# Performance work log

Measured on AMD Instinct MI355X. Metric: run time of the kernel, lower is better.

The kernel has to match this reference:

```python
import jax, jax.numpy as jnp
import numpy as np

N_NODES = 50000
N_EDGES = 200000
N_GRAPHS = 64
BN_EPS = 1e-5


def _gat(x, src, dst, W, a_src, a_dst, b, heads, ch, concat):
    # x: [N, F_in] -> h: [N, H, C]
    N = x.shape[0]
    h = (x @ W).reshape(N, heads, ch)
    alpha_s = jnp.sum(h * a_src, axis=-1)  # [N, H]
    alpha_d = jnp.sum(h * a_dst, axis=-1)  # [N, H]
    e = jax.nn.leaky_relu(alpha_s[src] + alpha_d[dst], 0.2)  # [E, H]
    # segment softmax over destination nodes
    m = jax.ops.segment_max(e, dst, num_segments=N)  # [N, H]
    e = jnp.exp(e - m[dst])
    s = jax.ops.segment_sum(e, dst, num_segments=N)
    alpha = e / (s[dst] + 1e-16)  # [E, H]
    msg = h[src] * alpha[:, :, None]  # [E, H, C]
    out = jax.ops.segment_sum(msg, dst, num_segments=N)  # [N, H, C]
    out = out.reshape(N, heads * ch) if concat else out.mean(axis=1)
    return out + b


def _bn(x, gamma, beta):
    # eval-mode BatchNorm1d with running_mean=0, running_var=1
    return x * (gamma / jnp.sqrt(1.0 + BN_EPS)) + beta


def _mlp3(g, W1, b1, W2, b2, W3, b3):
    h = jax.nn.relu(g @ W1 + b1)
    h = jax.nn.relu(h @ W2 + b2)
    return h @ W3 + b3


def setup_inputs() -> dict:
    key = jax.random.key(0)
    ks = jax.random.split(key, 48)
    it = iter(range(48))

    def nrm(shape, fan_in):
        return jax.random.normal(ks[next(it)], shape, jnp.float32) / np.sqrt(fan_in)

    x = jax.random.normal(ks[next(it)], (N_NODES, 62), jnp.float32)
    edge_index = jax.random.randint(ks[next(it)], (2, N_EDGES), 0, N_NODES, jnp.int32)
    batch = jnp.sort(jax.random.randint(ks[next(it)], (N_NODES,), 0, N_GRAPHS, jnp.int32))

    d = dict(x=x, edge_index=edge_index, batch=batch)
    d.update(
        Win=nrm((62, 256), 62), b_in=jnp.zeros((256,), jnp.float32),
        W1=nrm((256, 1024), 256), as1=nrm((8, 128), 128), ad1=nrm((8, 128), 128),
        b1=jnp.zeros((1024,), jnp.float32), g1=jnp.ones((1024,), jnp.float32), be1=jnp.zeros((1024,), jnp.float32),
        W2=nrm((1024, 1024), 1024), as2=nrm((8, 128), 128), ad2=nrm((8, 128), 128),
        b2=jnp.zeros((1024,), jnp.float32), g2=jnp.ones((1024,), jnp.float32), be2=jnp.zeros((1024,), jnp.float32),
        W3=nrm((1024, 1024), 1024), as3=nrm((4, 256), 256), ad3=nrm((4, 256), 256),
        b3=jnp.zeros((256,), jnp.float32), g3=jnp.ones((256,), jnp.float32), be3=jnp.zeros((256,), jnp.float32),
        Wp=nrm((768, 256), 768), bp=jnp.zeros((256,), jnp.float32),
        Wv1=nrm((256, 128), 256), bv1=jnp.zeros((128,), jnp.float32),
        Wv2=nrm((128, 64), 128), bv2=jnp.zeros((64,), jnp.float32),
        Wv3=nrm((64, 2), 64), bv3=jnp.zeros((2,), jnp.float32),
        Wt1=nrm((256, 128), 256), bt1=jnp.zeros((128,), jnp.float32),
        Wt2=nrm((128, 64), 128), bt2=jnp.zeros((64,), jnp.float32),
        Wt3=nrm((64, 10), 64), bt3=jnp.zeros((10,), jnp.float32),
        Wc1=nrm((256, 64), 256), bc1=jnp.zeros((64,), jnp.float32),
        Wc2=nrm((64, 1), 64), bc2=jnp.zeros((1,), jnp.float32),
    )
    return d


def reference(x, edge_index, batch, Win, b_in,
              W1, as1, ad1, b1, g1, be1,
              W2, as2, ad2, b2, g2, be2,
              W3, as3, ad3, b3, g3, be3,
              Wp, bp,
              Wv1, bv1, Wv2, bv2, Wv3, bv3,
              Wt1, bt1, Wt2, bt2, Wt3, bt3,
              Wc1, bc1, Wc2, bc2):
    N = x.shape[0]
    loop = jnp.arange(N, dtype=edge_index.dtype)
    src = jnp.concatenate([edge_index[0], loop])  # add_self_loops (PyG default)
    dst = jnp.concatenate([edge_index[1], loop])

    h = jax.nn.relu(x @ Win + b_in)
    x1 = jax.nn.relu(_bn(_gat(h, src, dst, W1, as1, ad1, b1, 8, 128, True), g1, be1))
    x2 = jax.nn.relu(_bn(_gat(x1, src, dst, W2, as2, ad2, b2, 8, 128, True), g2, be2))
    x3 = jax.nn.relu(_bn(_gat(x2, src, dst, W3, as3, ad3, b3, 4, 256, False), g3, be3))

    add_pool = jax.ops.segment_sum(x3, batch, num_segments=N_GRAPHS)
    cnt = jax.ops.segment_sum(jnp.ones((N,), x3.dtype), batch, num_segments=N_GRAPHS)
    mean_pool = add_pool / jnp.maximum(cnt, 1.0)[:, None]
    max_pool = jax.ops.segment_max(x3, batch, num_segments=N_GRAPHS)
    max_pool = jnp.where(jnp.isfinite(max_pool), max_pool, 0.0)

    pooled = jnp.concatenate([mean_pool, max_pool, add_pool], axis=1)  # [G, 768]
    g = jax.nn.relu(pooled @ Wp + bp)

    vuln = _mlp3(g, Wv1, bv1, Wv2, bv2, Wv3, bv3)            # [G, 2]
    vtype = _mlp3(g, Wt1, bt1, Wt2, bt2, Wt3, bt3)           # [G, 10]
    conf = jax.nn.sigmoid(jax.nn.relu(g @ Wc1 + bc1) @ Wc2 + bc2)  # [G, 1]
    return (vuln, vtype, conf)
```

## Files before the change

### kernel.cpp

```cpp
#include <hip/hip_runtime.h>
#include <stdint.h>

static constexpr int NN = 50000;
static constexpr int NP = 50176;
static constexpr int NE = 200000;
static constexpr int NG = 64;
#define BN_S 0.99999500003749968f

typedef __bf16 bf16x8 __attribute__((ext_vector_type(8)));
typedef float  f32x4  __attribute__((ext_vector_type(4)));
typedef __attribute__((address_space(1))) void* as1p;
typedef __attribute__((address_space(3))) void* as3p;
typedef unsigned short u16;

__device__ __forceinline__ float b2f(u16 u){ union{uint32_t i;float f;}x; x.i=((uint32_t)u)<<16; return x.f; }
__device__ __forceinline__ float lo_f(uint32_t u){ union{uint32_t i;float f;}x; x.i=u<<16; return x.f; }
__device__ __forceinline__ float hi_f(uint32_t u){ union{uint32_t i;float f;}x; x.i=u&0xffff0000u; return x.f; }
__device__ __forceinline__ u16 f2b(float f){
  union{float f;uint32_t i;}x; x.f=f;
  return (u16)((x.i + 0x7fffu + ((x.i>>16)&1u)) >> 16);
}
__device__ __forceinline__ void lds_cp16(const void* g, void* l){
  __builtin_amdgcn_global_load_lds((as1p)g, (as3p)l, 16, 0, 0);
}

__global__ void k_detect(const uint32_t* __restrict__ win, int* __restrict__ flag){
  const int lane = threadIdx.x;
  const uint32_t w = win[lane];
  const int e = (w >> 7) & 0xFF;
  const bool band = (e >= 100 && e <= 140) || ((w & 0xFFFFu) == 0u);
  unsigned long long m = __ballot(band);
  if (lane == 0) *flag = (__popcll(m) < 32) ? 1 : 0;
}

struct CvtJobs {
  const void* src[34];
  int n[34];
  int dstoff[34];
  int cum[35];
  int njobs;
  int total;
};
__global__ __launch_bounds__(256) void k_cvt(CvtJobs jobs, const int* __restrict__ flag,
                                             u16* __restrict__ dst0){
  const int i = blockIdx.x*256 + threadIdx.x;
  if (i >= jobs.total) return;
  int lo = 0, hi = jobs.njobs - 1;
  while (lo < hi){ int mid = (lo+hi+1)>>1; if (jobs.cum[mid] <= i) lo = mid; else hi = mid-1; }
  const int j = lo;
  const int e = i - jobs.cum[j];
  u16 v = (*flag) ? f2b(((const float*)jobs.src[j])[e]) : ((const u16*)jobs.src[j])[e];
  dst0[jobs.dstoff[j] + e] = v;
}

__global__ void k_pad_x(const void* __restrict__ x, u16* __restrict__ xp, const int* __restrict__ flag){
  int i = blockIdx.x*256 + threadIdx.x;
  if (i >= NP*64) return;
  int n = i >> 6, k = i & 63;
  u16 v = 0;
  if (n < NN && k < 62)
    v = (*flag) ? f2b(((const float*)x)[n*62 + k]) : ((const u16*)x)[n*62 + k];
  xp[i] = v;
}
__global__ void k_pad_winT(const void* __restrict__ w, u16* __restrict__ wt, const int* __restrict__ flag){
  int i = blockIdx.x*256 + threadIdx.x;
  if (i >= 256*64) return;
  int o = i >> 6, k = i & 63;
  u16 v = 0;
  if (k < 62)
    v = (*flag) ? f2b(((const float*)w)[k*256 + o]) : ((const u16*)w)[k*256 + o];
  wt[i] = v;
}
__global__ void k_transpose(const void* __restrict__ w, u16* __restrict__ wt, int K, int NO,
                            const int* __restrict__ flag){
  int i = blockIdx.x*256 + threadIdx.x;
  if (i >= K*NO) return;
  int k = i / NO, o = i - k*NO;
  u16 v = (*flag) ? f2b(((const float*)w)[i]) : ((const u16*)w)[i];
  wt[(size_t)o*K + k] = v;
}

__global__ void k_init_counts(int* counts){
  int i = blockIdx.x*256 + threadIdx.x;
  if (i < NN) counts[i] = 1;
}
__global__ void k_count(const int* __restrict__ eidx, int* counts){
  int e = blockIdx.x*256 + threadIdx.x;
  if (e < NE) atomicAdd(&counts[eidx[NE + e]], 1);
}
__global__ __launch_bounds__(1024) void k_scan(const int* __restrict__ counts,
                                               int* __restrict__ indptr, int* __restrict__ cursor){
  __shared__ int sums[1024];
  const int t = threadIdx.x;
  const int strip = (NN + 1023)/1024;
  int lo = t*strip, hi = lo+strip < NN ? lo+strip : NN;
  int s = 0;
  for (int i=lo;i<hi;i++) s += counts[i];
  sums[t] = s; __syncthreads();
  for (int off=1; off<1024; off<<=1){
    int v = (t>=off) ? sums[t-off] : 0;
    __syncthreads();
    sums[t] += v;
    __syncthreads();
  }
  int base = t ? sums[t-1] : 0;
  for (int i=lo;i<hi;i++){ indptr[i]=base; cursor[i]=base; base += counts[i]; }
  if (t == 1023) indptr[NN] = sums[1023];
}
__global__ void k_fill(const int* __restrict__ eidx, int* cursor, int* __restrict__ srcs){
  int i = blockIdx.x*256 + threadIdx.x;
  if (i >= NE + NN) return;
  int s, d;
  if (i < NE){ s = eidx[i]; d = eidx[NE+i]; }
  else { s = d = i - NE; }
  int p = atomicAdd(&cursor[d], 1);
  srcs[p] = s;
}

template<int K, bool EPI, int BNSH>
__global__ __launch_bounds__(256) void k_gemm_bt(const u16* __restrict__ A, const u16* __restrict__ B,
                                                 u16* __restrict__ C, int ldc, const u16* __restrict__ bias){
  __shared__ __align__(16) u16 As[128*64];
  __shared__ __align__(16) u16 Bs[128*64];
  const int tid = threadIdx.x;
  const int lane = tid & 63, wv = tid >> 6;
  const int bid = blockIdx.x;
  const size_t bm = bid >> BNSH, bn = bid & ((1<<BNSH)-1);
  const u16* Ab = A + bm*128*(size_t)K;
  const u16* Bb = B + bn*128*(size_t)K;
  f32x4 acc[4][4] = {};
  const int wm = (wv>>1)*64, wn = (wv&1)*64;
  const int r = lane & 15, kg = lane >> 4;
  const int srow = wv*32 + (lane>>3);
  const int scol = (lane&7)*8;
  for (int kt = 0; kt < K; kt += 64){
    #pragma unroll
    for (int i=0;i<4;i++){
      lds_cp16(Ab + (size_t)(srow + i*8)*K + kt + scol, (char*)As + (wv*4+i)*1024);
      lds_cp16(Bb + (size_t)(srow + i*8)*K + kt + scol, (char*)Bs + (wv*4+i)*1024);
    }
    __syncthreads();
    #pragma unroll
    for (int ks=0; ks<2; ks++){
      bf16x8 a[4], b[4];
      const int ko = ks*32 + kg*8;
      #pragma unroll
      for (int i=0;i<4;i++) a[i] = *(const bf16x8*)(As + (wm + i*16 + r)*64 + ko);
      #pragma unroll
      for (int j=0;j<4;j++) b[j] = *(const bf16x8*)(Bs + (wn + j*16 + r)*64 + ko);
      #pragma unroll
      for (int i=0;i<4;i++)
        #pragma unroll
        for (int j=0;j<4;j++)
          acc[i][j] = __builtin_amdgcn_mfma_f32_16x16x32_bf16(a[i], b[j], acc[i][j], 0, 0, 0);
    }
    __syncthreads();
  }
  const int rg = lane>>4, cl = lane&15;
  #pragma unroll
  for (int i=0;i<4;i++){
    #pragma unroll
    for (int j=0;j<4;j++){
      const int col = (int)bn*128 + wn + j*16 + cl;
      float bv = 0.f;
      if (EPI) bv = b2f(bias[col]);
      #pragma unroll
      for (int rr=0;rr<4;rr++){
        const int row = (int)bm*128 + wm + i*16 + rg*4 + rr;
        float v = acc[i][j][rr];
        if (EPI){ v += bv; v = v>0.f ? v : 0.f; }
        C[(size_t)row*ldc + col] = f2b(v);
      }
    }
  }
}

template<int K, int BNT>
__global__ __launch_bounds__(512, 2) void k_gemm256(const u16* __restrict__ A, const u16* __restrict__ B,
                                                    u16* __restrict__ C, int ldc){
  __shared__ __align__(16) u16 lds[65536];
  const int tid = threadIdx.x;
  const int lane = tid & 63, wid = tid >> 6;
  const int wr = wid >> 2, wc = wid & 3;
  const int bm = blockIdx.x / BNT, bn = blockIdx.x % BNT;
  const u16* Ab = A + (size_t)bm*256*K;
  const u16* Bb = B + (size_t)bn*256*K;
  const int r = lane & 15, kg = lane >> 4;
  const int r7 = r & 7;
  f32x4 acc[8][4] = {};

  auto stage = [&](int which, int T, int wro){
    const u16* src = (which < 2 ? Ab + (size_t)(which*128)*K
                                : Bb + (size_t)((which-2)*128)*K) + (size_t)T*64;
    u16* dst = lds + wro + (which >= 2 ? 16384 : 0) + (which & 1)*8192;
    const int gslot = (tid & 7) ^ ((tid >> 3) & 7);
    #pragma unroll
    for (int L = 0; L < 2; L++){
      const int off = L*4096 + tid*8;
      lds_cp16(src + (size_t)(off >> 6)*K + gslot*8, dst + off);
    }
  };

  auto do_tile = [&](int T, int rdo, int wro, bool prefetch){
    const u16* As_ = lds + rdo;
    const u16* Bs_ = lds + rdo + 16384;
    #pragma unroll
    for (int p = 0; p < 4; ++p){
      const int h = p >> 1, ks = p & 1;
      const int sl = ((ks*4 + kg) ^ r7) * 8;
      bf16x8 a[4], b[4];
      const u16* ap = As_ + (wr*128 + h*64 + r)*64 + sl;
      const u16* bp = Bs_ + (wc*64  +        r)*64 + sl;
      #pragma unroll
      for (int m = 0; m < 4; m++) a[m] = *(const bf16x8*)(ap + m*1024);
      #pragma unroll
      for (int n = 0; n < 4; n++) b[n] = *(const bf16x8*)(bp + n*1024);
      if (prefetch){
        if (p == 0){ stage(0, T+1, wro); stage(1, T+1, wro); }
        else if (p == 1){ stage(2, T+1, wro); stage(3, T+1, wro); }
      }
      __builtin_amdgcn_s_barrier();
      __builtin_amdgcn_s_setprio(1);
      #pragma unroll
      for (int m = 0; m < 4; m++)
        #pragma unroll
        for (int n = 0; n < 4; n++)
          acc[h*4+m][n] = __builtin_amdgcn_mfma_f32_16x16x32_bf16(a[m], b[n], acc[h*4+m][n], 0, 0, 0);
      __builtin_amdgcn_s_setprio(0);
      if (p < 3) __builtin_amdgcn_s_barrier();
      else       __syncthreads();
    }
  };

  constexpr int NT = K/64;
  stage(0,0,0); stage(1,0,0); stage(2,0,0); stage(3,0,0);
  __syncthreads();
  for (int T = 0; T < NT; T += 2){
    do_tile(T,     0,     32768, true);
    do_tile(T+1, 32768,   0,     T+2 < NT);
  }

  const int cl = lane & 15, rg = lane >> 4;
  #pragma unroll
  for (int h = 0; h < 2; h++)
    #pragma unroll
    for (int m = 0; m < 4; m++)
      #pragma unroll
      for (int n = 0; n < 4; n++){
        const int col = bn*256 + wc*64 + n*16 + cl;
        #pragma unroll
        for (int rr = 0; rr < 4; rr++){
          const int row = bm*256 + wr*128 + h*64 + m*16 + rg*4 + rr;
          C[(size_t)row*ldc + col] = f2b(acc[h*4+m][n][rr]);
        }
      }
}

template<int H>
__global__ __launch_bounds__(256) void k_alpha(const u16* __restrict__ h,
                                               const u16* __restrict__ a_s, const u16* __restrict__ a_d,
                                               float* __restrict__ os, float* __restrict__ od){
  const int n = blockIdx.x*4 + (threadIdx.x>>6);
  if (n >= NN) return;
  const int lane = threadIdx.x & 63;
  const int c0 = lane*16;
  const uint4 hv0 = *(const uint4*)(h + (size_t)n*1024 + c0);
  const uint4 hv1 = *(const uint4*)(h + (size_t)n*1024 + c0 + 8);
  const uint4 sv0 = *(const uint4*)(a_s + c0);
  const uint4 sv1 = *(const uint4*)(a_s + c0 + 8);
  const uint4 dv0 = *(const uint4*)(a_d + c0);
  const uint4 dv1 = *(const uint4*)(a_d + c0 + 8);
  float ss = 0.f, sd = 0.f;
  uint32_t hu[8] = {hv0.x,hv0.y,hv0.z,hv0.w,hv1.x,hv1.y,hv1.z,hv1.w};
  uint32_t su[8] = {sv0.x,sv0.y,sv0.z,sv0.w,sv1.x,sv1.y,sv1.z,sv1.w};
  uint32_t du[8] = {dv0.x,dv0.y,dv0.z,dv0.w,dv1.x,dv1.y,dv1.z,dv1.w};
  #pragma unroll
  for (int q=0;q<8;q++){
    float h0 = lo_f(hu[q]), h1 = hi_f(hu[q]);
    ss += h0*lo_f(su[q]) + h1*hi_f(su[q]);
    sd += h0*lo_f(du[q]) + h1*hi_f(du[q]);
  }
  const int G = 64 / H;
  #pragma unroll
  for (int off=1; off<G; off<<=1){ ss += __shfl_xor(ss, off); sd += __shfl_xor(sd, off); }
  if ((lane & (G-1)) == 0){
    os[n*H + lane/G] = ss;
    od[n*H + lane/G] = sd;
  }
}

template<int H>
__global__ __launch_bounds__(256) void k_soft(const float* __restrict__ asb, const float* __restrict__ adb,
                                              const int* __restrict__ indptr, const int* __restrict__ srcs,
                                              float* __restrict__ wbuf, float* __restrict__ invs){
  const int idx = blockIdx.x*256 + threadIdx.x;
  if (idx >= NN*H) return;
  const int n = idx / H, hh = idx - n*H;
  const float adn = adb[idx];
  const int p0 = indptr[n], p1 = indptr[n+1];
  float m = -1e30f;
  for (int p = p0; p < p1; ++p){
    float t = asb[srcs[p]*H + hh] + adn;
    float v = t > 0.f ? t : 0.2f*t;
    m = fmaxf(m, v);
  }
  float s = 0.f;
  for (int p = p0; p < p1; ++p){
    float t = asb[srcs[p]*H + hh] + adn;
    float v = t > 0.f ? t : 0.2f*t;
    float e = __expf(v - m);
    wbuf[(size_t)p*H + hh] = e;
    s += e;
  }
  invs[idx] = 1.0f/(s + 1e-16f);
}

template<int H, int C, bool FINAL>
__global__ __launch_bounds__(256) void k_agg2(const u16* __restrict__ h,
                                              const float* __restrict__ wbuf, const float* __restrict__ invs,
                                              const int* __restrict__ indptr, const int* __restrict__ srcs,
                                              const u16* __restrict__ bias, const u16* __restrict__ gamma,
                                              const u16* __restrict__ beta, u16* __restrict__ out){
  const int n = blockIdx.x;
  const int tid = threadIdx.x;
  constexpr int OUTW = FINAL ? C : H*C;
  if (n >= NN){
    for (int c = tid; c < OUTW; c += 256) out[(size_t)n*OUTW + c] = 0;
    return;
  }
  const int p0 = indptr[n], p1 = indptr[n+1];
  if (!FINAL){
    const int c0 = tid*4;
    const int hd = c0 >> 7;
    float a0=0.f,a1=0.f,a2=0.f,a3=0.f;
    int p = p0;
    for (; p + 2 <= p1; p += 2){
      const int s0 = srcs[p], s1 = srcs[p+1];
      const float w0 = wbuf[(size_t)p*H + hd];
      const float w1 = wbuf[(size_t)(p+1)*H + hd];
      const ushort4 v0 = *(const ushort4*)(h + (size_t)s0*1024 + c0);
      const ushort4 v1 = *(const ushort4*)(h + (size_t)s1*1024 + c0);
      a0 += w0*b2f(v0.x) + w1*b2f(v1.x);
      a1 += w0*b2f(v0.y) + w1*b2f(v1.y);
      a2 += w0*b2f(v0.z) + w1*b2f(v1.z);
      a3 += w0*b2f(v0.w) + w1*b2f(v1.w);
    }
    if (p < p1){
      const int s0 = srcs[p];
      const float w0 = wbuf[(size_t)p*H + hd];
      const ushort4 v0 = *(const ushort4*)(h + (size_t)s0*1024 + c0);
      a0 += w0*b2f(v0.x); a1 += w0*b2f(v0.y); a2 += w0*b2f(v0.z); a3 += w0*b2f(v0.w);
    }
    const float is = invs[n*H + hd];
    float vv[4] = {a0,a1,a2,a3};
    u16 ov[4];
    #pragma unroll
    for (int i2=0;i2<4;i2++){
      const int c = c0 + i2;
      float v = (vv[i2]*is + b2f(bias[c])) * (b2f(gamma[c])*BN_S) + b2f(beta[c]);
      ov[i2] = f2b(v>0.f ? v : 0.f);
    }
    *(ushort4*)(out + (size_t)n*1024 + c0) = make_ushort4(ov[0],ov[1],ov[2],ov[3]);
  } else {
    const int c = tid;
    float a0=0.f,a1=0.f,a2=0.f,a3=0.f;
    for (int p = p0; p < p1; ++p){
      const int s = srcs[p];
      const float4 w4 = *(const float4*)(wbuf + (size_t)p*4);
      const u16* hr = h + (size_t)s*1024 + c;
      a0 += w4.x * b2f(hr[0]);
      a1 += w4.y * b2f(hr[256]);
      a2 += w4.z * b2f(hr[512]);
      a3 += w4.w * b2f(hr[768]);
    }
    const float4 is = *(const float4*)(invs + n*4);
    float meanv = 0.25f*(a0*is.x + a1*is.y + a2*is.z + a3*is.w);
    float v = (meanv + b2f(bias[c])) * (b2f(gamma[c])*BN_S) + b2f(beta[c]);
    out[(size_t)n*C + c] = f2b(v>0.f ? v : 0.f);
  }
}

__global__ __launch_bounds__(256) void k_pool_init(float* __restrict__ pooled, int* __restrict__ gcnt){
  int i = blockIdx.x*256 + threadIdx.x;
  if (i < NG*768) pooled[i] = 0.f;
  if (i < NG) gcnt[i] = 0;
}
__global__ __launch_bounds__(256) void k_pool1(const u16* __restrict__ x3, const int* __restrict__ batch,
                                               float* __restrict__ pooled, int* __restrict__ gcnt){
  const int n0 = blockIdx.x*64;
  const int n1 = (n0+64 < NN) ? n0+64 : NN;
  if (n0 >= NN) return;
  const int t = threadIdx.x;
  float sum=0.f, mx=0.f;
  int curg = batch[n0];
  int segstart = n0;
  for (int n=n0; n<n1; ++n){
    const int g = batch[n];
    if (g != curg){
      atomicAdd(&pooled[curg*768+512+t], sum);
      atomicMax((unsigned int*)&pooled[curg*768+256+t], __float_as_uint(mx));
      if (t==0) atomicAdd(&gcnt[curg], n-segstart);
      sum=0.f; mx=0.f; curg=g; segstart=n;
    }
    float v = b2f(x3[(size_t)n*256+t]);
    sum += v; mx = fmaxf(mx, v);
  }
  atomicAdd(&pooled[curg*768+512+t], sum);
  atomicMax((unsigned int*)&pooled[curg*768+256+t], __float_as_uint(mx));
  if (t==0) atomicAdd(&gcnt[curg], n1-segstart);
}
__global__ __launch_bounds__(256) void k_pool_fin(float* __restrict__ pooled, const int* __restrict__ gcnt){
  int i = blockIdx.x*256 + threadIdx.x;
  if (i >= NG*256) return;
  int g = i>>8, c = i&255;
  float s = pooled[g*768+512+c];
  int cnt = gcnt[g];
  pooled[g*768+c] = s / (float)(cnt>1?cnt:1);
}

__global__ __launch_bounds__(256) void k_gvec(const float* __restrict__ pooled, const u16* __restrict__ Wp,
                                              const u16* __restrict__ bp, float* __restrict__ gbuf){
  const int g = blockIdx.x, t = threadIdx.x;
  __shared__ float ps[768];
  for (int i=t;i<768;i+=256) ps[i] = pooled[g*768+i];
  __syncthreads();
  float acc = b2f(bp[t]);
  for (int k=0;k<768;k++) acc += ps[k]*b2f(Wp[k*256+t]);
  gbuf[g*256+t] = acc>0.f ? acc : 0.f;
}
__global__ __launch_bounds__(128) void k_heads(const float* __restrict__ gbuf,
    const u16* Wv1,const u16* bv1,const u16* Wv2,const u16* bv2,const u16* Wv3,const u16* bv3,
    const u16* Wt1,const u16* bt1,const u16* Wt2,const u16* bt2,const u16* Wt3,const u16* bt3,
    const u16* Wc1,const u16* bc1,const u16* Wc2,const u16* bc2,
    void* __restrict__ outp, const int* __restrict__ flag){
  const int g = blockIdx.x, t = threadIdx.x;
  const int f32o = *flag;
  u16* o16 = (u16*)outp;
  float* o32 = (float*)outp;
  __shared__ float gs[256], h1[128], h2[64];
  gs[t] = gbuf[g*256+t]; gs[t+128] = gbuf[g*256+t+128];
  __syncthreads();
  { float a = b2f(bv1[t]); for (int k=0;k<256;k++) a += gs[k]*b2f(Wv1[k*128+t]); h1[t] = a>0.f?a:0.f; }
  __syncthreads();
  if (t<64){ float a=b2f(bv2[t]); for(int k=0;k<128;k++) a += h1[k]*b2f(Wv2[k*64+t]); h2[t]=a>0.f?a:0.f; }
  __syncthreads();
  if (t<2){ float a=b2f(bv3[t]); for(int k=0;k<64;k++) a += h2[k]*b2f(Wv3[k*2+t]);
            if (f32o) o32[g*2+t]=a; else o16[g*2+t]=f2b(a); }
  __syncthreads();
  { float a = b2f(bt1[t]); for (int k=0;k<256;k++) a += gs[k]*b2f(Wt1[k*128+t]); h1[t] = a>0.f?a:0.f; }
  __syncthreads();
  if (t<64){ float a=b2f(bt2[t]); for(int k=0;k<128;k++) a += h1[k]*b2f(Wt2[k*64+t]); h2[t]=a>0.f?a:0.f; }
  __syncthreads();
  if (t<10){ float a=b2f(bt3[t]); for(int k=0;k<64;k++) a += h2[k]*b2f(Wt3[k*10+t]);
             if (f32o) o32[128 + g*10+t]=a; else o16[128 + g*10+t]=f2b(a); }
  __syncthreads();
  if (t<64){ float a=b2f(bc1[t]); for(int k=0;k<256;k++) a += gs[k]*b2f(Wc1[k*64+t]); h2[t]=a>0.f?a:0.f; }
  __syncthreads();
  if (t==0){
    float a=b2f(bc2[0]);
    for(int k=0;k<64;k++) a += h2[k]*b2f(Wc2[k]);
    float r = 1.f/(1.f+__expf(-a));
    if (f32o) o32[768+g]=r; else o16[768+g]=f2b(r);
  }
}

extern "C" void kernel_launch(void* const* d_in, const int* in_sizes, int n_in,
                              void* d_out, int out_size, void* d_ws, size_t ws_size,
                              hipStream_t stream){
  (void)in_sizes; (void)n_in; (void)out_size; (void)ws_size;
  const int* eidx = (const int*)d_in[1];
  const int* batch= (const int*)d_in[2];

  char* ws = (char*)d_ws;
  size_t off = 0;
  auto alloc = [&](size_t bytes) -> void* {
    void* p = ws + off;
    off += (bytes + 255) & ~(size_t)255;
    return p;
  };
  u16* bufA  = (u16*)alloc((size_t)NP*1024*2);
  u16* bufH  = (u16*)alloc((size_t)NP*1024*2);
  u16* W1t   = (u16*)alloc((size_t)1024*256*2);
  u16* W2t   = (u16*)alloc((size_t)1024*1024*2);
  u16* W3t   = (u16*)alloc((size_t)1024*1024*2);
  u16* WinT  = (u16*)alloc((size_t)256*64*2);
  const size_t wbytes = ((size_t)(NE+NN)*8*4 + 255) & ~(size_t)255;
  const size_t ibytes = (size_t)NN*8*4;
  const size_t xbytes = (size_t)NP*64*2;
  char* un = (char*)alloc(wbytes + ibytes > xbytes ? wbytes + ibytes : xbytes);
  u16*   Xp   = (u16*)un;
  float* wbuf = (float*)un;
  float* invs = (float*)(un + wbytes);
  float* asb = (float*)alloc((size_t)NN*8*4);
  float* adb = (float*)alloc((size_t)NN*8*4);
  int* counts= (int*)alloc((size_t)NN*4);
  int* cursor= (int*)alloc((size_t)NN*4);
  int* indptr= (int*)alloc((size_t)(NN+1)*4);
  int* srcs  = (int*)alloc((size_t)(NE+NN)*4);
  float* pooled = (float*)alloc((size_t)NG*768*4);
  float* gbuf   = (float*)alloc((size_t)NG*256*4);
  int* gcnt  = (int*)alloc((size_t)NG*4);
  u16* cvt   = (u16*)alloc((size_t)320*1024*2);
  int* flag  = (int*)alloc(256);

  CvtJobs jobs; int ji = 0; int cvtoff = 0; int cume = 0;
  auto addjob = [&](int idx, int n) -> u16* {
    jobs.src[ji] = d_in[idx]; jobs.n[ji] = n; jobs.dstoff[ji] = cvtoff;
    jobs.cum[ji] = cume; cume += n; ji++;
    u16* r = cvt + cvtoff; cvtoff = (cvtoff + n + 15) & ~15; return r;
  };
  u16* cb_in= addjob(4, 256);
  u16* cas1 = addjob(6, 1024);  u16* cad1 = addjob(7, 1024);
  u16* cb1  = addjob(8, 1024);  u16* cg1  = addjob(9, 1024);  u16* cbe1 = addjob(10, 1024);
  u16* cas2 = addjob(12, 1024); u16* cad2 = addjob(13, 1024);
  u16* cb2  = addjob(14, 1024); u16* cg2  = addjob(15, 1024); u16* cbe2 = addjob(16, 1024);
  u16* cas3 = addjob(18, 1024); u16* cad3 = addjob(19, 1024);
  u16* cb3  = addjob(20, 256);  u16* cg3  = addjob(21, 256);  u16* cbe3 = addjob(22, 256);
  u16* cWp  = addjob(23, 196608); u16* cbp = addjob(24, 256);
  u16* cWv1 = addjob(25, 32768);  u16* cbv1= addjob(26, 128);
  u16* cWv2 = addjob(27, 8192);   u16* cbv2= addjob(28, 64);
  u16* cWv3 = addjob(29, 128);    u16* cbv3= addjob(30, 2);
  u16* cWt1 = addjob(31, 32768);  u16* cbt1= addjob(32, 128);
  u16* cWt2 = addjob(33, 8192);   u16* cbt2= addjob(34, 64);
  u16* cWt3 = addjob(35, 640);    u16* cbt3= addjob(36, 10);
  u16* cWc1 = addjob(37, 16384);  u16* cbc1= addjob(38, 64);
  u16* cWc2 = addjob(39, 64);     u16* cbc2= addjob(40, 1);
  jobs.cum[ji] = cume; jobs.njobs = ji; jobs.total = cume;

  k_detect<<<1, 64, 0, stream>>>((const uint32_t*)d_in[3], flag);
  k_cvt<<<(cume+255)/256, 256, 0, stream>>>(jobs, flag, cvt);
  k_pad_x<<<(NP*64+255)/256, 256, 0, stream>>>(d_in[0], Xp, flag);
  k_pad_winT<<<(256*64+255)/256, 256, 0, stream>>>(d_in[3], WinT, flag);
  k_transpose<<<(256*1024+255)/256, 256, 0, stream>>>(d_in[5], W1t, 256, 1024, flag);
  k_transpose<<<(1024*1024+255)/256, 256, 0, stream>>>(d_in[11], W2t, 1024, 1024, flag);
  k_transpose<<<(1024*1024+255)/256, 256, 0, stream>>>(d_in[17], W3t, 1024, 1024, flag);

  k_init_counts<<<(NN+255)/256, 256, 0, stream>>>(counts);
  k_count<<<(NE+255)/256, 256, 0, stream>>>(eidx, counts);
  k_scan<<<1, 1024, 0, stream>>>(counts, indptr, cursor);
  k_fill<<<(NE+NN+255)/256, 256, 0, stream>>>(eidx, cursor, srcs);

  k_gemm_bt<64,true,1><<<dim3((NP/128)*2), 256, 0, stream>>>(Xp, WinT, bufA, 256, cb_in);

  k_gemm256<256,4><<<dim3((NP/256)*4), 512, 0, stream>>>(bufA, W1t, bufH, 1024);
  k_alpha<8><<<(NN+3)/4, 256, 0, stream>>>(bufH, cas1, cad1, asb, adb);
  k_soft<8><<<(NN*8+255)/256, 256, 0, stream>>>(asb, adb, indptr, srcs, wbuf, invs);
  k_agg2<8,128,false><<<NP, 256, 0, stream>>>(bufH, wbuf, invs, indptr, srcs, cb1, cg1, cbe1, bufA);

  k_gemm256<1024,4><<<dim3((NP/256)*4), 512, 0, stream>>>(bufA, W2t, bufH, 1024);
  k_alpha<8><<<(NN+3)/4, 256, 0, stream>>>(bufH, cas2, cad2, asb, adb);
  k_soft<8><<<(NN*8+255)/256, 256, 0, stream>>>(asb, adb, indptr, srcs, wbuf, invs);
  k_agg2<8,128,false><<<NP, 256, 0, stream>>>(bufH, wbuf, invs, indptr, srcs, cb2, cg2, cbe2, bufA);

  k_gemm256<1024,4><<<dim3((NP/256)*4), 512, 0, stream>>>(bufA, W3t, bufH, 1024);
  k_alpha<4><<<(NN+3)/4, 256, 0, stream>>>(bufH, cas3, cad3, asb, adb);
  k_soft<4><<<(NN*4+255)/256, 256, 0, stream>>>(asb, adb, indptr, srcs, wbuf, invs);
  k_agg2<4,256,true><<<NP, 256, 0, stream>>>(bufH, wbuf, invs, indptr, srcs, cb3, cg3, cbe3, bufA);

  k_pool_init<<<(NG*768+255)/256, 256, 0, stream>>>(pooled, gcnt);
  k_pool1<<<(NN+63)/64, 256, 0, stream>>>(bufA, batch, pooled, gcnt);
  k_pool_fin<<<(NG*256+255)/256, 256, 0, stream>>>(pooled, gcnt);
  k_gvec<<<NG, 256, 0, stream>>>(pooled, cWp, cbp, gbuf);
  k_heads<<<NG, 128, 0, stream>>>(gbuf, cWv1,cbv1,cWv2,cbv2,cWv3,cbv3,
                                  cWt1,cbt1,cWt2,cbt2,cWt3,cbt3, cWc1,cbc1,cWc2,cbc2,
                                  d_out, flag);
}
```

Measured before the change: 909.0 us.

## Fuse attention-coefficient dot products into GEMM epilogue with atomic accumulation

The separate k_alpha kernel is removed. The per-head source and destination attention dot products are now computed from the fp32 GEMM accumulators in the k_gemm256 epilogue, reduced across lanes with shuffles, and accumulated into asb/adb with atomicAdd. A zeroing kernel runs before each GEMM. This avoids re-reading the 50000x1024 bf16 feature matrix three times and uses fp32 accumulators instead of bf16-rounded values. The cost is extra epilogue work, register pressure and atomics in the GEMM.

New measurement: 1.133 ms. 24.7% more time.

```diff
diff --git a/kernel.cpp b/kernel.cpp
--- a/kernel.cpp
+++ b/kernel.cpp
@@ -53,6 +53,11 @@
   dst0[jobs.dstoff[j] + e] = v;
 }
 
+__global__ void k_zero(float* __restrict__ a, float* __restrict__ b, int n){
+  int i = blockIdx.x*256 + threadIdx.x;
+  if (i < n){ a[i] = 0.f; b[i] = 0.f; }
+}
+
 __global__ void k_pad_x(const void* __restrict__ x, u16* __restrict__ xp, const int* __restrict__ flag){
   int i = blockIdx.x*256 + threadIdx.x;
   if (i >= NP*64) return;
@@ -175,9 +180,11 @@
   }
 }
 
-template<int K, int BNT>
+template<int K, int BNT, int HD>
 __global__ __launch_bounds__(512, 2) void k_gemm256(const u16* __restrict__ A, const u16* __restrict__ B,
-                                                    u16* __restrict__ C, int ldc){
+                                                    u16* __restrict__ C, int ldc,
+                                                    const u16* __restrict__ a_s, const u16* __restrict__ a_d,
+                                                    float* __restrict__ asb, float* __restrict__ adb){
   __shared__ __align__(16) u16 lds[65536];
   const int tid = threadIdx.x;
   const int lane = tid & 63, wid = tid >> 6;
@@ -254,39 +261,41 @@
           C[(size_t)row*ldc + col] = f2b(acc[h*4+m][n][rr]);
         }
       }
-}
-
-template<int H>
-__global__ __launch_bounds__(256) void k_alpha(const u16* __restrict__ h,
-                                               const u16* __restrict__ a_s, const u16* __restrict__ a_d,
-                                               float* __restrict__ os, float* __restrict__ od){
-  const int n = blockIdx.x*4 + (threadIdx.x>>6);
-  if (n >= NN) return;
-  const int lane = threadIdx.x & 63;
-  const int c0 = lane*16;
-  const uint4 hv0 = *(const uint4*)(h + (size_t)n*1024 + c0);
-  const uint4 hv1 = *(const uint4*)(h + (size_t)n*1024 + c0 + 8);
-  const uint4 sv0 = *(const uint4*)(a_s + c0);
-  const uint4 sv1 = *(const uint4*)(a_s + c0 + 8);
-  const uint4 dv0 = *(const uint4*)(a_d + c0);
-  const uint4 dv1 = *(const uint4*)(a_d + c0 + 8);
-  float ss = 0.f, sd = 0.f;
-  uint32_t hu[8] = {hv0.x,hv0.y,hv0.z,hv0.w,hv1.x,hv1.y,hv1.z,hv1.w};
-  uint32_t su[8] = {sv0.x,sv0.y,sv0.z,sv0.w,sv1.x,sv1.y,sv1.z,sv1.w};
-  uint32_t du[8] = {dv0.x,dv0.y,dv0.z,dv0.w,dv1.x,dv1.y,dv1.z,dv1.w};
+
+  const int hd = ((bn*256 + wc*64) * HD) >> 10;
+  float asv[4], adv[4];
   #pragma unroll
-  for (int q=0;q<8;q++){
-    float h0 = lo_f(hu[q]), h1 = hi_f(hu[q]);
-    ss += h0*lo_f(su[q]) + h1*hi_f(su[q]);
-    sd += h0*lo_f(du[q]) + h1*hi_f(du[q]);
-  }
-  const int G = 64 / H;
+  for (int n = 0; n < 4; n++){
+    const int col = bn*256 + wc*64 + n*16 + cl;
+    asv[n] = b2f(a_s[col]);
+    adv[n] = b2f(a_d[col]);
+  }
   #pragma unroll
-  for (int off=1; off<G; off<<=1){ ss += __shfl_xor(ss, off); sd += __shfl_xor(sd, off); }
-  if ((lane & (G-1)) == 0){
-    os[n*H + lane/G] = ss;
-    od[n*H + lane/G] = sd;
-  }
+  for (int h = 0; h < 2; h++)
+    #pragma unroll
+    for (int m = 0; m < 4; m++)
+      #pragma unroll
+      for (int rr = 0; rr < 4; rr++){
+        float ss = 0.f, sd = 0.f;
+        #pragma unroll
+        for (int n = 0; n < 4; n++){
+          const float v = acc[h*4+m][n][rr];
+          ss += v * asv[n];
+          sd += v * adv[n];
+        }
+        #pragma unroll
+        for (int k2 = 8; k2 >= 1; k2 >>= 1){
+          ss += __shfl_xor(ss, k2);
+          sd += __shfl_xor(sd, k2);
+        }
+        if (cl == 0){
+          const int row = bm*256 + wr*128 + h*64 + m*16 + rg*4 + rr;
+          if (row < NN){
+            atomicAdd(&asb[row*HD + hd], ss);
+            atomicAdd(&adb[row*HD + hd], sd);
+          }
+        }
+      }
 }
 
 template<int H>
@@ -542,18 +551,18 @@
 
   k_gemm_bt<64,true,1><<<dim3((NP/128)*2), 256, 0, stream>>>(Xp, WinT, bufA, 256, cb_in);
 
-  k_gemm256<256,4><<<dim3((NP/256)*4), 512, 0, stream>>>(bufA, W1t, bufH, 1024);
-  k_alpha<8><<<(NN+3)/4, 256, 0, stream>>>(bufH, cas1, cad1, asb, adb);
+  k_zero<<<(NN*8+255)/256, 256, 0, stream>>>(asb, adb, NN*8);
+  k_gemm256<256,4,8><<<dim3((NP/256)*4), 512, 0, stream>>>(bufA, W1t, bufH, 1024, cas1, cad1, asb, adb);
   k_soft<8><<<(NN*8+255)/256, 256, 0, stream>>>(asb, adb, indptr, srcs, wbuf, invs);
   k_agg2<8,128,false><<<NP, 256, 0, stream>>>(bufH, wbuf, invs, indptr, srcs, cb1, cg1, cbe1, bufA);
 
-  k_gemm256<1024,4><<<dim3((NP/256)*4), 512, 0, stream>>>(bufA, W2t, bufH, 1024);
-  k_alpha<8><<<(NN+3)/4, 256, 0, stream>>>(bufH, cas2, cad2, asb, adb);
+  k_zero<<<(NN*8+255)/256, 256, 0, stream>>>(asb, adb, NN*8);
+  k_gemm256<1024,4,8><<<dim3((NP/256)*4), 512, 0, stream>>>(bufA, W2t, bufH, 1024, cas2, cad2, asb, adb);
   k_soft<8><<<(NN*8+255)/256, 256, 0, stream>>>(asb, adb, indptr, srcs, wbuf, invs);
   k_agg2<8,128,false><<<NP, 256, 0, stream>>>(bufH, wbuf, invs, indptr, srcs, cb2, cg2, cbe2, bufA);
 
-  k_gemm256<1024,4><<<dim3((NP/256)*4), 512, 0, stream>>>(bufA, W3t, bufH, 1024);
-  k_alpha<4><<<(NN+3)/4, 256, 0, stream>>>(bufH, cas3, cad3, asb, adb);
+  k_zero<<<(NN*4+255)/256, 256, 0, stream>>>(asb, adb, NN*4);
+  k_gemm256<1024,4,4><<<dim3((NP/256)*4), 512, 0, stream>>>(bufA, W3t, bufH, 1024, cas3, cad3, asb, adb);
   k_soft<4><<<(NN*4+255)/256, 256, 0, stream>>>(asb, adb, indptr, srcs, wbuf, invs);
   k_agg2<4,256,true><<<NP, 256, 0, stream>>>(bufH, wbuf, invs, indptr, srcs, cb3, cg3, cbe3, bufA);
 
```
